# Kernel optimization log

Measured on AMD Instinct MI355X. Metric: run time of the kernel, lower is better.

The kernel has to match this reference:

```python
import jax, jax.numpy as jnp
import numpy as np

CODEBOOK_SIZE = 1024
CODEBOOK_DIM = 64
COMMITMENT_COST = 0.25


def setup_inputs() -> dict:
    key = jax.random.key(0)
    k_in, k_cb = jax.random.split(key)
    inputs = jax.random.normal(k_in, (64, 64, 64, CODEBOOK_DIM), dtype=jnp.float32)
    # nn.init.uniform_(weight, -1/K, 1/K)
    codebook = jax.random.uniform(
        k_cb, (CODEBOOK_SIZE, CODEBOOK_DIM), dtype=jnp.float32,
        minval=-1.0 / CODEBOOK_SIZE, maxval=1.0 / CODEBOOK_SIZE)
    return {"inputs": inputs, "codebook": codebook}


def reference(inputs, codebook):
    K, D = codebook.shape
    flat = inputs.reshape(-1, D)  # (N, D)
    distances = (
        jnp.sum(flat * flat, axis=-1, keepdims=True)
        - 2.0 * (flat @ codebook.T)
        + jnp.sum(codebook * codebook, axis=-1)[None, :]
    )
    idx = jnp.argmin(distances, axis=-1)  # (N,)
    codes = jnp.take(codebook, idx, axis=0).reshape(inputs.shape)
    # commitment loss (quantize detached)
    commitment_loss = jnp.mean(jnp.square(jax.lax.stop_gradient(codes) - inputs))
    loss = COMMITMENT_COST * commitment_loss
    # straight-through estimator
    quantize = inputs + jax.lax.stop_gradient(codes - inputs)
    # perplexity via cluster counts (equivalent to one_hot.mean(0), no NxK one-hot)
    counts = jax.ops.segment_sum(
        jnp.ones(idx.shape, dtype=inputs.dtype), idx, num_segments=K)
    avg_probs = counts / jnp.asarray(idx.shape[0], dtype=inputs.dtype)
    perplexity = jnp.exp(-jnp.sum(avg_probs * jnp.log(avg_probs + 1e-10)))
    return quantize, loss, perplexity
```

## Files before the change

kernel.cpp:

```cpp
#include <hip/hip_runtime.h>

#define NVEC (64*64*64)
#define KCB 1024
#define DIM 64
#define VB 128
#define BATCHES 8
#define GRID 256
#define NSLOT 32

typedef __attribute__((ext_vector_type(8))) short s16x8;
typedef __attribute__((ext_vector_type(4))) float f32x4;

#define MFMA16(A, B, C) __builtin_amdgcn_mfma_f32_16x16x32_bf16((A), (B), (C), 0, 0, 0)

#define LDS_BARRIER()                                        \
    do {                                                     \
        asm volatile("s_waitcnt lgkmcnt(0)" ::: "memory");   \
        __builtin_amdgcn_s_barrier();                        \
        asm volatile("" ::: "memory");                       \
    } while (0)


__global__ __launch_bounds__(256) void vq_prep(const float* __restrict__ cb,
                                               unsigned short* __restrict__ cbA,
                                               float* __restrict__ cnf,
                                               unsigned int* __restrict__ slots) {
    int q = blockIdx.x * 256 + threadIdx.x;
    ((int4*)slots)[q] = int4{0, 0, 0, 0};
    int t = q >> 7;
    int h = (q >> 6) & 1;
    int l = q & 63;
    int m = t * 16 + (l & 15);
    int d0 = h * 32 + ((l >> 4) & 3) * 8;
    const float* row = cb + (size_t)m * DIM + d0;
    unsigned short* dst = cbA + (size_t)q * 8;
    #pragma unroll
    for (int j = 0; j < 8; ++j) {
        float f = -2.0f * row[j];
        unsigned u = __float_as_uint(f);
        dst[j] = (unsigned short)((u + 0x7fffu + ((u >> 16) & 1u)) >> 16);
    }
    if (q < KCB) {
        const float* r2 = cb + (size_t)q * DIM;
        double s = 0.0;
        for (int d = 0; d < DIM; ++d) { double c = (double)r2[d]; s = fma(c, c, s); }
        cnf[q] = (float)s;
    }
}

__global__ __launch_bounds__(1024) void vq_main(const float* __restrict__ inp,
                                                const unsigned short* __restrict__ cbA,
                                                const float* __restrict__ cnf,
                                                const float* __restrict__ cb,
                                                float* __restrict__ out,
                                                float* __restrict__ partials,
                                                unsigned int* __restrict__ slots) {
    __shared__ unsigned short xf[2][1024][8];
    __shared__ float xnp[2][1024];
    __shared__ float sred[VB][17];
    __shared__ unsigned int histS[KCB];
    __shared__ float lossL[64];

    const int tid  = threadIdx.x;
    const int lane = tid & 63;
    const int wv   = tid >> 6;
    const int l15  = lane & 15;
    const int g    = lane >> 4;
    const int gi   = g * 4;
    const int blockbase = blockIdx.x * (BATCHES * VB);

    const int cvt_vt    = tid >> 7;
    const int cvt_h     = (tid >> 6) & 1;
    const int cvt_l     = tid & 63;
    const int cvt_vec   = cvt_vt * 16 + (cvt_l & 15);
    const int cvt_d0    = cvt_h * 32 + (cvt_l >> 4) * 8;
    const int cvt_slice = cvt_h * 4 + (cvt_l >> 4);

    histS[tid] = 0u;

    float4 x0, x1;
    {
        const float* xp = inp + (size_t)(blockbase + cvt_vec) * DIM + cvt_d0;
        x0 = ((const float4*)xp)[0];
        x1 = ((const float4*)xp)[1];
    }

    const s16x8* __restrict__ Ap = (const s16x8*)cbA;
    s16x8 A[4][2];
    f32x4 cn[4];
    #pragma unroll
    for (int tt = 0; tt < 4; ++tt) {
        int T = wv * 4 + tt;
        A[tt][0] = Ap[(T * 2 + 0) * 64 + lane];
        A[tt][1] = Ap[(T * 2 + 1) * 64 + lane];
        cn[tt]   = *(const f32x4*)(cnf + T * 16 + gi);
    }

    float loss_acc = 0.0f;

    for (int b = 0; b < BATCHES; ++b) {
        const int buf = b & 1;
        const int vecbase = blockbase + b * VB;

        {
            float f[8] = {x0.x, x0.y, x0.z, x0.w, x1.x, x1.y, x1.z, x1.w};
            float xn = 0.f;
            unsigned wq[4];
            #pragma unroll
            for (int p = 0; p < 4; ++p) {
                xn = fmaf(f[2*p], f[2*p], xn);
                xn = fmaf(f[2*p+1], f[2*p+1], xn);
                unsigned r;
                asm("v_cvt_pk_bf16_f32 %0, %1, %2" : "=v"(r) : "v"(f[2*p]), "v"(f[2*p+1]));
                wq[p] = r;
            }
            *(int4*)&xf[buf][tid][0] = *(const int4*)wq;
            xnp[buf][cvt_vec * 8 + cvt_slice] = xn;
        }
        LDS_BARRIER();

        if (b + 1 < BATCHES) {
            const float* xp = inp + (size_t)(vecbase + VB + cvt_vec) * DIM + cvt_d0;
            x0 = ((const float4*)xp)[0];
            x1 = ((const float4*)xp)[1];
        }

        float bestv[8];
        #pragma unroll
        for (int vt = 0; vt < 8; ++vt) {
            s16x8 xb0 = *(const s16x8*)&xf[buf][(vt * 2 + 0) * 64 + lane][0];
            s16x8 xb1 = *(const s16x8*)&xf[buf][(vt * 2 + 1) * 64 + lane][0];
            f32x4 a0 = cn[0], a1 = cn[1], a2 = cn[2], a3 = cn[3];
            a0 = MFMA16(A[0][0], xb0, a0);
            a1 = MFMA16(A[1][0], xb0, a1);
            a2 = MFMA16(A[2][0], xb0, a2);
            a3 = MFMA16(A[3][0], xb0, a3);
            a0 = MFMA16(A[0][1], xb1, a0);
            a1 = MFMA16(A[1][1], xb1, a1);
            a2 = MFMA16(A[2][1], xb1, a2);
            a3 = MFMA16(A[3][1], xb1, a3);

            float bv = 3.4e38f;
            #define PACKMIN(ACC, TT) {                                                        \
                unsigned cbase = (unsigned)(wv * 64 + (TT) * 16 + gi);                        \
                float p0 = __uint_as_float((__float_as_uint(ACC[0]) & 0xFFFFFC00u) | cbase);  \
                float p1 = __uint_as_float((__float_as_uint(ACC[1]) & 0xFFFFFC00u) | (cbase+1));\
                float p2 = __uint_as_float((__float_as_uint(ACC[2]) & 0xFFFFFC00u) | (cbase+2));\
                float p3 = __uint_as_float((__float_as_uint(ACC[3]) & 0xFFFFFC00u) | (cbase+3));\
                float m01;                                                                    \
                asm("v_min3_f32 %0, %1, %2, %3" : "=v"(m01) : "v"(p0), "v"(p1), "v"(p2));     \
                asm("v_min3_f32 %0, %1, %2, %3" : "=v"(bv) : "v"(m01), "v"(p3), "v"(bv)); }
            PACKMIN(a0, 0) PACKMIN(a1, 1) PACKMIN(a2, 2) PACKMIN(a3, 3)
            #undef PACKMIN
            bestv[vt] = bv;
        }

        #pragma unroll
        for (int vt = 0; vt < 8; ++vt) {
            bestv[vt] = fminf(bestv[vt], __shfl_xor(bestv[vt], 16));
            bestv[vt] = fminf(bestv[vt], __shfl_xor(bestv[vt], 32));
        }
        if (g == 0) {
            #pragma unroll
            for (int vt = 0; vt < 8; ++vt) sred[vt * 16 + l15][wv] = bestv[vt];
        }
        LDS_BARRIER();

        #pragma unroll
        for (int rep = 0; rep < 2; ++rep) {
            const int vec = rep * 64 + (tid >> 4), sl = tid & 15;
            float pb = sred[vec][sl];
            pb = fminf(pb, __shfl_xor(pb, 1));
            pb = fminf(pb, __shfl_xor(pb, 2));
            pb = fminf(pb, __shfl_xor(pb, 4));
            pb = fminf(pb, __shfl_xor(pb, 8));
            int bk = (int)(__float_as_uint(pb) & 1023u);
            float4 q = ((const float4*)cb)[bk * 16 + sl];
            ((float4*)out)[(size_t)(vecbase + vec) * 16 + sl] = q;
            if (sl == 0) {
                float xn = 0.f;
                #pragma unroll
                for (int j = 0; j < 8; ++j) xn += xnp[buf][vec * 8 + j];
                loss_acc += pb + xn;
                atomicAdd(&histS[bk], 1u);
            }
        }
    }

    if ((tid & 15) == 0) lossL[tid >> 4] = loss_acc;
    __syncthreads();
    if (tid < 64) {
        float v = lossL[tid];
        #pragma unroll
        for (int off = 32; off > 0; off >>= 1) v += __shfl_xor(v, off);
        if (tid == 0) partials[blockIdx.x] = v;
    }
    unsigned hv = histS[tid];
    if (hv) atomicAdd(&slots[(blockIdx.x & (NSLOT - 1)) * KCB + tid], hv);
}

__global__ __launch_bounds__(1024) void vq_finalize(float* __restrict__ out,
                                                    const float* __restrict__ partials,
                                                    const unsigned int* __restrict__ slots) {
    __shared__ double red[1024];
    const int tid = threadIdx.x;
    unsigned tot = 0;
    #pragma unroll
    for (int s = 0; s < NSLOT; ++s) tot += slots[s * KCB + tid];
    double p = (double)tot / (double)NVEC;
    double h = p * log(p + 1e-10);
    double ls = (tid < GRID) ? (double)partials[tid] : 0.0;

    red[tid] = ls;
    __syncthreads();
    for (int t = 512; t > 0; t >>= 1) {
        if (tid < t) red[tid] += red[tid + t];
        __syncthreads();
    }
    double loss_tot = red[0];
    __syncthreads();
    red[tid] = h;
    __syncthreads();
    for (int t = 512; t > 0; t >>= 1) {
        if (tid < t) red[tid] += red[tid + t];
        __syncthreads();
    }
    if (tid == 0) {
        out[(size_t)NVEC * DIM]     = (float)(0.25 * loss_tot / (double)((size_t)NVEC * DIM));
        out[(size_t)NVEC * DIM + 1] = (float)exp(-red[0]);
    }
}

extern "C" void kernel_launch(void* const* d_in, const int* in_sizes, int n_in,
                              void* d_out, int out_size, void* d_ws, size_t ws_size,
                              hipStream_t stream) {
    const float* inp = (const float*)d_in[0];
    const float* cb  = (const float*)d_in[1];
    float* out = (float*)d_out;

    char* ws = (char*)d_ws;
    float*          cnf      = (float*)(ws + 0);
    unsigned short* cbA      = (unsigned short*)(ws + 4096);
    float*          partials = (float*)(ws + 135168);
    unsigned int*   slots    = (unsigned int*)(ws + 137216);

    vq_prep<<<dim3(32), dim3(256), 0, stream>>>(cb, cbA, cnf, slots);
    vq_main<<<dim3(GRID), dim3(1024), 0, stream>>>(inp, cbA, cnf, cb, out,
                                                   partials, slots);
    vq_finalize<<<dim3(1), dim3(1024), 0, stream>>>(out, partials, slots);
}
```

Measured before the change: 58.23 us.

## Software-pipeline batch conversion into epilogue and cut one barrier per batch

Converts the next batch's inputs to bf16 before the first barrier of the current batch's epilogue, so each batch uses one LDS barrier instead of two. The argmin reduction table is double-buffered to allow this. The epilogue is remapped to 8 threads per vector handling two float4 each, and the squared norm is reduced with shuffles rather than an 8-element LDS loop. MFMA sections get raised wave priority, and the final loss reduction is reworked. In exchange it uses more LDS and keeps more values live in registers.

```diff
diff --git a/kernel.cpp b/kernel.cpp
--- a/kernel.cpp
+++ b/kernel.cpp
@@ -57,7 +57,7 @@
                                                 unsigned int* __restrict__ slots) {
     __shared__ unsigned short xf[2][1024][8];
     __shared__ float xnp[2][1024];
-    __shared__ float sred[VB][17];
+    __shared__ float sred[2][VB][17];
     __shared__ unsigned int histS[KCB];
     __shared__ float lossL[64];
 
@@ -76,6 +76,9 @@
     const int cvt_d0    = cvt_h * 32 + (cvt_l >> 4) * 8;
     const int cvt_slice = cvt_h * 4 + (cvt_l >> 4);
 
+    const int evec = tid >> 3;
+    const int sl8  = tid & 7;
+
     histS[tid] = 0u;
 
     float4 x0, x1;
@@ -96,28 +99,28 @@
         cn[tt]   = *(const f32x4*)(cnf + T * 16 + gi);
     }
 
+    {
+        float f[8] = {x0.x, x0.y, x0.z, x0.w, x1.x, x1.y, x1.z, x1.w};
+        float xn = 0.f;
+        unsigned wq[4];
+        #pragma unroll
+        for (int p = 0; p < 4; ++p) {
+            xn = fmaf(f[2*p], f[2*p], xn);
+            xn = fmaf(f[2*p+1], f[2*p+1], xn);
+            unsigned r;
+            asm("v_cvt_pk_bf16_f32 %0, %1, %2" : "=v"(r) : "v"(f[2*p]), "v"(f[2*p+1]));
+            wq[p] = r;
+        }
+        *(int4*)&xf[0][tid][0] = *(const int4*)wq;
+        xnp[0][cvt_vec * 8 + cvt_slice] = xn;
+    }
+    LDS_BARRIER();
+
     float loss_acc = 0.0f;
 
     for (int b = 0; b < BATCHES; ++b) {
         const int buf = b & 1;
         const int vecbase = blockbase + b * VB;
-
-        {
-            float f[8] = {x0.x, x0.y, x0.z, x0.w, x1.x, x1.y, x1.z, x1.w};
-            float xn = 0.f;
-            unsigned wq[4];
-            #pragma unroll
-            for (int p = 0; p < 4; ++p) {
-                xn = fmaf(f[2*p], f[2*p], xn);
-                xn = fmaf(f[2*p+1], f[2*p+1], xn);
-                unsigned r;
-                asm("v_cvt_pk_bf16_f32 %0, %1, %2" : "=v"(r) : "v"(f[2*p]), "v"(f[2*p+1]));
-                wq[p] = r;
-            }
-            *(int4*)&xf[buf][tid][0] = *(const int4*)wq;
-            xnp[buf][cvt_vec * 8 + cvt_slice] = xn;
-        }
-        LDS_BARRIER();
 
         if (b + 1 < BATCHES) {
             const float* xp = inp + (size_t)(vecbase + VB + cvt_vec) * DIM + cvt_d0;
@@ -125,6 +128,7 @@
             x1 = ((const float4*)xp)[1];
         }
 
+        __builtin_amdgcn_s_setprio(1);
         float bestv[8];
         #pragma unroll
         for (int vt = 0; vt < 8; ++vt) {
@@ -154,6 +158,7 @@
             #undef PACKMIN
             bestv[vt] = bv;
         }
+        __builtin_amdgcn_s_setprio(0);
 
         #pragma unroll
         for (int vt = 0; vt < 8; ++vt) {
@@ -162,38 +167,63 @@
         }
         if (g == 0) {
             #pragma unroll
-            for (int vt = 0; vt < 8; ++vt) sred[vt * 16 + l15][wv] = bestv[vt];
-        }
+            for (int vt = 0; vt < 8; ++vt) sred[buf][vt * 16 + l15][wv] = bestv[vt];
+        }
+
+        float xn_reg = xnp[buf][tid];
+        xn_reg += __shfl_xor(xn_reg, 1);
+        xn_reg += __shfl_xor(xn_reg, 2);
+        xn_reg += __shfl_xor(xn_reg, 4);
+
+        if (b + 1 < BATCHES) {
+            float f[8] = {x0.x, x0.y, x0.z, x0.w, x1.x, x1.y, x1.z, x1.w};
+            float xn = 0.f;
+            unsigned wq[4];
+            #pragma unroll
+            for (int p = 0; p < 4; ++p) {
+                xn = fmaf(f[2*p], f[2*p], xn);
+                xn = fmaf(f[2*p+1], f[2*p+1], xn);
+                unsigned r;
+                asm("v_cvt_pk_bf16_f32 %0, %1, %2" : "=v"(r) : "v"(f[2*p]), "v"(f[2*p+1]));
+                wq[p] = r;
+            }
+            *(int4*)&xf[buf ^ 1][tid][0] = *(const int4*)wq;
+            xnp[buf ^ 1][cvt_vec * 8 + cvt_slice] = xn;
+        }
+
         LDS_BARRIER();
 
-        #pragma unroll
-        for (int rep = 0; rep < 2; ++rep) {
-            const int vec = rep * 64 + (tid >> 4), sl = tid & 15;
-            float pb = sred[vec][sl];
+        {
+            float pb = fminf(sred[buf][evec][sl8], sred[buf][evec][sl8 + 8]);
             pb = fminf(pb, __shfl_xor(pb, 1));
             pb = fminf(pb, __shfl_xor(pb, 2));
             pb = fminf(pb, __shfl_xor(pb, 4));
-            pb = fminf(pb, __shfl_xor(pb, 8));
             int bk = (int)(__float_as_uint(pb) & 1023u);
-            float4 q = ((const float4*)cb)[bk * 16 + sl];
-            ((float4*)out)[(size_t)(vecbase + vec) * 16 + sl] = q;
-            if (sl == 0) {
-                float xn = 0.f;
-                #pragma unroll
-                for (int j = 0; j < 8; ++j) xn += xnp[buf][vec * 8 + j];
-                loss_acc += pb + xn;
+            const float4* cr = (const float4*)cb + (size_t)bk * 16;
+            float4 q0 = cr[sl8];
+            float4 q1 = cr[sl8 + 8];
+            float4* ov = (float4*)out + (size_t)(vecbase + evec) * 16;
+            ov[sl8]     = q0;
+            ov[sl8 + 8] = q1;
+            if (sl8 == 0) {
+                loss_acc += pb + xn_reg;
                 atomicAdd(&histS[bk], 1u);
             }
         }
     }
 
-    if ((tid & 15) == 0) lossL[tid >> 4] = loss_acc;
-    __syncthreads();
-    if (tid < 64) {
-        float v = lossL[tid];
-        #pragma unroll
-        for (int off = 32; off > 0; off >>= 1) v += __shfl_xor(v, off);
-        if (tid == 0) partials[blockIdx.x] = v;
+    if ((tid & 7) == 0) lossL[tid >> 4] = 0.f;
+    __syncthreads();
+    float lw = loss_acc;
+    #pragma unroll
+    for (int off = 32; off > 0; off >>= 1) lw += __shfl_xor(lw, off);
+    if (lane == 0) lossL[wv] = lw;
+    __syncthreads();
+    if (tid == 0) {
+        float v = 0.f;
+        #pragma unroll
+        for (int i = 0; i < 16; ++i) v += lossL[i];
+        partials[blockIdx.x] = v;
     }
     unsigned hv = histS[tid];
     if (hv) atomicAdd(&slots[(blockIdx.x & (NSLOT - 1)) * KCB + tid], hv);
```

New measurement: 56.41 us. -3.1%, faster.
